# Kernel tuning notes

Measured on AMD Instinct MI355X. Metric: run time of the kernel, lower is better.

## Reference

```python
import jax, jax.numpy as jnp
import numpy as np

TEMPERATURE = 0.5


def setup_inputs() -> dict:
    key = jax.random.key(0)
    k1, k2 = jax.random.split(key)
    N, D = 4096, 512
    emb_i = jax.random.normal(k1, (N, D), dtype=jnp.float32)
    emb_j = jax.random.normal(k2, (N, D), dtype=jnp.float32)
    return {"emb_i": emb_i, "emb_j": emb_j}


def reference(emb_i, emb_j):
    # L2-normalize each embedding row (F.normalize, dim=1)
    z_i = emb_i / jnp.linalg.norm(emb_i, axis=1, keepdims=True)
    z_j = emb_j / jnp.linalg.norm(emb_j, axis=1, keepdims=True)
    reps = jnp.concatenate([z_i, z_j], axis=0)  # [2N, D]
    N = emb_i.shape[0]
    M = 2 * N
    # cosine similarity of normalized vectors == dot product -> [2N, 2N]
    sim = jnp.einsum('id,jd->ij', reps, reps) / TEMPERATURE
    # denominator: sum_k!=i exp(sim[i,k]); original multiplies by one-hot complement
    exp_sim = jnp.exp(sim)
    denom = jnp.sum(exp_sim, axis=1) - jnp.diagonal(exp_sim)  # [2N]
    log_denom = jnp.log(denom)
    # positive pairs: (k, k+N) and (k+N, k)
    idx = jnp.arange(N)
    pos_ij = sim[idx, idx + N]          # sim(k, k+N)/T
    pos_ji = sim[idx + N, idx]          # sim(k+N, k)/T
    loss = jnp.sum(-(pos_ij - log_denom[:N]) - (pos_ji - log_denom[N:]))
    return loss / (2.0 * N)
```

## Files before the change

kernel.cpp:

```cpp
#include <hip/hip_runtime.h>
#include <cstdint>
#include <cstddef>

constexpr int N_ROWS = 4096;
constexpr int D      = 512;
constexpr int M      = 8192;
constexpr int NTILE  = 64;
constexpr int NBLK   = NTILE * (NTILE + 1) / 2;
constexpr int BKB    = 64;
constexpr int NKT    = D / BKB;
constexpr int LDSB   = 128 * BKB;

using f32x16 = __attribute__((ext_vector_type(16))) float;
using i32x4  = __attribute__((ext_vector_type(4))) int;
using i32x8  = __attribute__((ext_vector_type(8))) int;
using ul2    = __attribute__((ext_vector_type(2))) unsigned long;

#define ASYNC_CP16(gsrc, ldst)                                                      \
    __builtin_amdgcn_global_load_lds(                                               \
        (const __attribute__((address_space(1))) unsigned int*)(gsrc),              \
        (__attribute__((address_space(3))) unsigned int*)(ldst), 16, 0, 0)

#define SS_FP8(pk, accum)                                                           \
    do {                                                                            \
        float f0 = __builtin_amdgcn_cvt_f32_fp8((pk), 0);                           \
        float f1 = __builtin_amdgcn_cvt_f32_fp8((pk), 1);                           \
        float f2 = __builtin_amdgcn_cvt_f32_fp8((pk), 2);                           \
        float f3 = __builtin_amdgcn_cvt_f32_fp8((pk), 3);                           \
        (accum) += f0 * f0 + f1 * f1 + f2 * f2 + f3 * f3;                           \
    } while (0)

__global__ __launch_bounds__(256) void normpos_kernel(
    const float* __restrict__ emb_i, const float* __restrict__ emb_j,
    uint8_t* __restrict__ zb, float* __restrict__ diagss,
    float* __restrict__ pos)
{
    const int wave = threadIdx.x >> 6, lane = threadIdx.x & 63;
    const int k = blockIdx.x * 4 + wave;

    const float4* a = (const float4*)(emb_i + (size_t)k * D);
    const float4* b = (const float4*)(emb_j + (size_t)k * D);
    float4 a0 = a[lane * 2], a1 = a[lane * 2 + 1];
    float4 b0 = b[lane * 2], b1 = b[lane * 2 + 1];

    float ssi = a0.x*a0.x + a0.y*a0.y + a0.z*a0.z + a0.w*a0.w
              + a1.x*a1.x + a1.y*a1.y + a1.z*a1.z + a1.w*a1.w;
    float ssj = b0.x*b0.x + b0.y*b0.y + b0.z*b0.z + b0.w*b0.w
              + b1.x*b1.x + b1.y*b1.y + b1.z*b1.z + b1.w*b1.w;
    float dp  = a0.x*b0.x + a0.y*b0.y + a0.z*b0.z + a0.w*b0.w
              + a1.x*b1.x + a1.y*b1.y + a1.z*b1.z + a1.w*b1.w;
    #pragma unroll
    for (int off = 32; off; off >>= 1) {
        ssi += __shfl_xor(ssi, off, 64);
        ssj += __shfl_xor(ssj, off, 64);
        dp  += __shfl_xor(dp,  off, 64);
    }
    const float invi = rsqrtf(ssi), invj = rsqrtf(ssj);

    const float zi[8] = {a0.x*invi, a0.y*invi, a0.z*invi, a0.w*invi,
                         a1.x*invi, a1.y*invi, a1.z*invi, a1.w*invi};
    const float zj[8] = {b0.x*invj, b0.y*invj, b0.z*invj, b0.w*invj,
                         b1.x*invj, b1.y*invj, b1.z*invj, b1.w*invj};

    int pi0 = __builtin_amdgcn_cvt_pk_fp8_f32(zi[0], zi[1], 0, false);
    pi0     = __builtin_amdgcn_cvt_pk_fp8_f32(zi[2], zi[3], pi0, true);
    int pi1 = __builtin_amdgcn_cvt_pk_fp8_f32(zi[4], zi[5], 0, false);
    pi1     = __builtin_amdgcn_cvt_pk_fp8_f32(zi[6], zi[7], pi1, true);
    int pj0 = __builtin_amdgcn_cvt_pk_fp8_f32(zj[0], zj[1], 0, false);
    pj0     = __builtin_amdgcn_cvt_pk_fp8_f32(zj[2], zj[3], pj0, true);
    int pj1 = __builtin_amdgcn_cvt_pk_fp8_f32(zj[4], zj[5], 0, false);
    pj1     = __builtin_amdgcn_cvt_pk_fp8_f32(zj[6], zj[7], pj1, true);

    float dssi = 0.f, dssj = 0.f;
    SS_FP8(pi0, dssi);
    SS_FP8(pi1, dssi);
    SS_FP8(pj0, dssj);
    SS_FP8(pj1, dssj);

    const int x   = (k >> 1) & 3;
    const int sl8 = (lane >> 3) * 8 + ((((lane >> 1) & 3) ^ x) * 2) + (lane & 1);
    const unsigned long long vi =
        ((unsigned long long)(unsigned)pi1 << 32) | (unsigned)pi0;
    const unsigned long long vj =
        ((unsigned long long)(unsigned)pj1 << 32) | (unsigned)pj0;
    *(unsigned long long*)(zb + (size_t)k * D + sl8 * 8)            = vi;
    *(unsigned long long*)(zb + (size_t)(k + N_ROWS) * D + sl8 * 8) = vj;

    #pragma unroll
    for (int off = 32; off; off >>= 1) {
        dssi += __shfl_xor(dssi, off, 64);
        dssj += __shfl_xor(dssj, off, 64);
    }
    if (lane == 0) {
        diagss[k]          = dssi;
        diagss[k + N_ROWS] = dssj;
        pos[k]             = 2.0f * dp * invi * invj;
    }
}

__global__ __launch_bounds__(256, 4) void simgemm_kernel(
    const uint8_t* __restrict__ zb, float* __restrict__ partials)
{
    __shared__ ul2 AsV[2 * LDSB / 16];
    __shared__ ul2 BsV[2 * LDSB / 16];
    __shared__ float rp[4][64];
    __shared__ float cp4[4][64];
    uint8_t* As = (uint8_t*)AsV;
    uint8_t* Bs = (uint8_t*)BsV;

    const int tid  = threadIdx.x;
    const int wave = tid >> 6, lane = tid & 63;
    const int l31  = lane & 31, half = lane >> 5;

    const int t = blockIdx.x;
    int bi = (int)((129.0f - sqrtf(129.0f * 129.0f - 8.0f * (float)t)) * 0.5f);
    while (bi > 0 && bi * (129 - bi) / 2 > t) --bi;
    while ((bi + 1) * (129 - (bi + 1)) / 2 <= t) ++bi;
    const int bj = bi + (t - bi * (129 - bi) / 2);
    const bool diag = (bi == bj);

    const int wrow = (wave >> 1) * 64, wcol = (wave & 1) * 64;

    const int srow = wave * 32 + (lane >> 2);
    const int scol = (lane & 3) * 16;
    const uint8_t* gA = zb + (size_t)(bi * 128 + srow) * D + scol;
    const uint8_t* gB = zb + (size_t)(bj * 128 + srow) * D + scol;
    uint8_t* lA = As + wave * 32 * BKB;
    uint8_t* lB = Bs + wave * 32 * BKB;

#define STAGE4(IT)                                                                  \
    do {                                                                            \
        const int _kc  = (IT) * BKB;                                                \
        const int _off = ((IT) & 1) * LDSB;                                         \
        ASYNC_CP16(gA + _kc,          lA + _off);                                   \
        ASYNC_CP16(gA + _kc + 16 * D, lA + _off + 16 * BKB);                        \
        ASYNC_CP16(gB + _kc,          lB + _off);                                   \
        ASYNC_CP16(gB + _kc + 16 * D, lB + _off + 16 * BKB);                        \
    } while (0)

    STAGE4(0);

    f32x16 acc[2][2] = {};
    const int c0b = ((2 * half) ^ ((l31 >> 1) & 3)) * 16;

    #pragma unroll
    for (int it = 0; it < NKT; ++it) {
        __builtin_amdgcn_s_barrier();
        asm volatile("" ::: "memory");

        if (it + 1 < NKT) {
            STAGE4(it + 1);
            asm volatile("s_waitcnt vmcnt(4)" ::: "memory");
        } else {
            asm volatile("s_waitcnt vmcnt(0)" ::: "memory");
        }
        __builtin_amdgcn_s_barrier();
        asm volatile("" ::: "memory");

        const int cb = (it & 1) * LDSB;
        i32x8 af[2], bf[2];
        #pragma unroll
        for (int f = 0; f < 2; ++f) {
            const uint8_t* pa = As + cb + (size_t)(wrow + f * 32 + l31) * BKB;
            i32x4 alo = *(const i32x4*)(pa + c0b);
            i32x4 ahi = *(const i32x4*)(pa + (c0b ^ 16));
            af[f] = __builtin_shufflevector(alo, ahi, 0, 1, 2, 3, 4, 5, 6, 7);
            const uint8_t* pb = Bs + cb + (size_t)(wcol + f * 32 + l31) * BKB;
            i32x4 blo = *(const i32x4*)(pb + c0b);
            i32x4 bhi = *(const i32x4*)(pb + (c0b ^ 16));
            bf[f] = __builtin_shufflevector(blo, bhi, 0, 1, 2, 3, 4, 5, 6, 7);
        }
        #pragma unroll
        for (int i = 0; i < 2; ++i)
            #pragma unroll
            for (int j = 0; j < 2; ++j)
                acc[i][j] = __builtin_amdgcn_mfma_scale_f32_32x32x64_f8f6f4(
                    af[i], bf[j], acc[i][j], 0, 0,
                    0, 0x7f7f7f7f, 0, 0x7f7f7f7f);
    }

    float rowp[2][16] = {};
    #pragma unroll
    for (int j = 0; j < 2; ++j) {
        float cpj = 0.f;
        #pragma unroll
        for (int i = 0; i < 2; ++i)
            #pragma unroll
            for (int r = 0; r < 16; ++r) {
                float e = __expf(2.0f * acc[i][j][r]);
                rowp[i][r] += e;
                cpj += e;
            }
        if (!diag) {
            cpj += __shfl_xor(cpj, 32, 64);
            if (half == 0) cp4[wave][j * 32 + l31] = cpj;
        }
    }
    #pragma unroll
    for (int i = 0; i < 2; ++i)
        #pragma unroll
        for (int r = 0; r < 16; ++r) {
            float e = rowp[i][r];
            e += __shfl_xor(e, 1, 64);
            e += __shfl_xor(e, 2, 64);
            e += __shfl_xor(e, 4, 64);
            e += __shfl_xor(e, 8, 64);
            e += __shfl_xor(e, 16, 64);
            if (l31 == 0)
                rp[wave][i * 32 + (r & 3) + 8 * (r >> 2) + 4 * half] = e;
        }
    __syncthreads();

    float* pA = partials + (size_t)(bi * NTILE + bj) * 128;
    float* pB = partials + (size_t)(bj * NTILE + bi) * 128;
    if (tid < 128) {
        const int h = tid >> 6, rr = tid & 63;
        pA[tid] = rp[h * 2][rr] + rp[h * 2 + 1][rr];
    } else if (!diag) {
        const int c = tid - 128, h = c >> 6, cc = c & 63;
        pB[c] = cp4[h][cc] + cp4[h + 2][cc];
    }
}

__global__ __launch_bounds__(256) void rowfin_kernel(
    const float* __restrict__ partials, const float* __restrict__ diagss,
    const float* __restrict__ pos, float* __restrict__ lgpart)
{
    const int r  = blockIdx.x;
    const int ri = threadIdx.x & 127;
    const int ch = threadIdx.x >> 7;
    const float* base = partials + (size_t)r * NTILE * 128 + ri;
    float s = 0.f;
    #pragma unroll
    for (int c = 0; c < 32; ++c)
        s += base[(size_t)(ch * 32 + c) * 128];
    __shared__ float half1[128];
    __shared__ float red[4];
    if (ch == 1) half1[ri] = s;
    __syncthreads();
    float lg = 0.f;
    if (ch == 0) {
        float rs = s + half1[ri];
        int row = r * 128 + ri;
        lg = __logf(rs - __expf(2.0f * diagss[row]));
    }
    if (threadIdx.x < 64)
        lg -= 2.0f * pos[r * 64 + threadIdx.x];
    #pragma unroll
    for (int off = 32; off; off >>= 1) lg += __shfl_xor(lg, off, 64);
    const int wave = threadIdx.x >> 6, lane = threadIdx.x & 63;
    if (lane == 0) red[wave] = lg;
    __syncthreads();
    if (threadIdx.x == 0) lgpart[r] = red[0] + red[1] + red[2] + red[3];
}

__global__ __launch_bounds__(64) void loss_kernel(
    const float* __restrict__ lgpart, float* __restrict__ out)
{
    float local = lgpart[threadIdx.x];
    #pragma unroll
    for (int off = 32; off; off >>= 1) local += __shfl_xor(local, off, 64);
    if (threadIdx.x == 0) out[0] = local * (1.0f / 8192.0f);
}

extern "C" void kernel_launch(void* const* d_in, const int* in_sizes, int n_in,
                              void* d_out, int out_size, void* d_ws, size_t ws_size,
                              hipStream_t stream)
{
    const float* emb_i = (const float*)d_in[0];
    const float* emb_j = (const float*)d_in[1];

    uint8_t* zb = (uint8_t*)d_ws;
    float* partials = (float*)((char*)d_ws + (size_t)M * D);
    float* diagss   = partials + (size_t)NTILE * NTILE * 128;
    float* pos      = diagss + M;
    float* lgpart   = pos + N_ROWS;
    float* out      = (float*)d_out;

    normpos_kernel<<<N_ROWS / 4, 256, 0, stream>>>(emb_i, emb_j, zb, diagss, pos);
    simgemm_kernel<<<NBLK, 256, 0, stream>>>(zb, partials);
    rowfin_kernel<<<NTILE, 256, 0, stream>>>(partials, diagss, pos, lgpart);
    loss_kernel<<<1, 64, 0, stream>>>(lgpart, out);
}
```

Baseline: 110.9 us.

## Enlarge similarity GEMM tiles to 256x256 with 8-wave blocks

The symmetric FP8 similarity GEMM moves from 128x128 upper-triangle tiles with 4 waves to 256x256 tiles with 8 waves, each wave computing a 128x64 sub-tile. Larger tiles halve global/LDS traffic per output and cut the block count from 2080 to 528. To keep the existing rowfin partial layout, each 256-wide row sum goes into one 128-column slot and the paired slot is zeroed. The tradeoffs are higher register and LDS use, a 2-block-per-CU occupancy target, and fewer blocks, which may give a coarser tail across CUs.

```diff
diff --git a/kernel.cpp b/kernel.cpp
--- a/kernel.cpp
+++ b/kernel.cpp
@@ -6,10 +6,11 @@
 constexpr int D      = 512;
 constexpr int M      = 8192;
 constexpr int NTILE  = 64;
-constexpr int NBLK   = NTILE * (NTILE + 1) / 2;
+constexpr int NT2    = 32;
+constexpr int NJOB2  = NT2 * (NT2 + 1) / 2;
 constexpr int BKB    = 64;
 constexpr int NKT    = D / BKB;
-constexpr int LDSB   = 128 * BKB;
+constexpr int TBY    = 256 * BKB;
 
 using f32x16 = __attribute__((ext_vector_type(16))) float;
 using i32x4  = __attribute__((ext_vector_type(4))) int;
@@ -98,13 +99,13 @@
     }
 }
 
-__global__ __launch_bounds__(256, 4) void simgemm_kernel(
+__global__ __launch_bounds__(512, 2) void simgemm_kernel(
     const uint8_t* __restrict__ zb, float* __restrict__ partials)
 {
-    __shared__ ul2 AsV[2 * LDSB / 16];
-    __shared__ ul2 BsV[2 * LDSB / 16];
-    __shared__ float rp[4][64];
-    __shared__ float cp4[4][64];
+    __shared__ ul2 AsV[2 * TBY / 16];
+    __shared__ ul2 BsV[2 * TBY / 16];
+    __shared__ float rp[8][128];
+    __shared__ float cp[8][64];
     uint8_t* As = (uint8_t*)AsV;
     uint8_t* Bs = (uint8_t*)BsV;
 
@@ -113,25 +114,28 @@
     const int l31  = lane & 31, half = lane >> 5;
 
     const int t = blockIdx.x;
-    int bi = (int)((129.0f - sqrtf(129.0f * 129.0f - 8.0f * (float)t)) * 0.5f);
-    while (bi > 0 && bi * (129 - bi) / 2 > t) --bi;
-    while ((bi + 1) * (129 - (bi + 1)) / 2 <= t) ++bi;
-    const int bj = bi + (t - bi * (129 - bi) / 2);
+    int bi = (int)((65.0f - sqrtf(4225.0f - 8.0f * (float)t)) * 0.5f);
+    if (bi < 0) bi = 0;
+    if (bi > 31) bi = 31;
+    while (bi > 0 && bi * (65 - bi) / 2 > t) --bi;
+    while ((bi + 1) * (65 - (bi + 1)) / 2 <= t) ++bi;
+    const int bj = bi + (t - bi * (65 - bi) / 2);
     const bool diag = (bi == bj);
 
-    const int wrow = (wave >> 1) * 64, wcol = (wave & 1) * 64;
+    const int wr = wave >> 2, wc = wave & 3;
+    const int wrow = wr * 128, wcol = wc * 64;
 
     const int srow = wave * 32 + (lane >> 2);
     const int scol = (lane & 3) * 16;
-    const uint8_t* gA = zb + (size_t)(bi * 128 + srow) * D + scol;
-    const uint8_t* gB = zb + (size_t)(bj * 128 + srow) * D + scol;
+    const uint8_t* gA = zb + (size_t)(bi * 256 + srow) * D + scol;
+    const uint8_t* gB = zb + (size_t)(bj * 256 + srow) * D + scol;
     uint8_t* lA = As + wave * 32 * BKB;
     uint8_t* lB = Bs + wave * 32 * BKB;
 
 #define STAGE4(IT)                                                                  \
     do {                                                                            \
         const int _kc  = (IT) * BKB;                                                \
-        const int _off = ((IT) & 1) * LDSB;                                         \
+        const int _off = ((IT) & 1) * TBY;                                          \
         ASYNC_CP16(gA + _kc,          lA + _off);                                   \
         ASYNC_CP16(gA + _kc + 16 * D, lA + _off + 16 * BKB);                        \
         ASYNC_CP16(gB + _kc,          lB + _off);                                   \
@@ -140,7 +144,7 @@
 
     STAGE4(0);
 
-    f32x16 acc[2][2] = {};
+    f32x16 acc[4][2] = {};
     const int c0b = ((2 * half) ^ ((l31 >> 1) & 3)) * 16;
 
     #pragma unroll
@@ -157,21 +161,24 @@
         __builtin_amdgcn_s_barrier();
         asm volatile("" ::: "memory");
 
-        const int cb = (it & 1) * LDSB;
-        i32x8 af[2], bf[2];
-        #pragma unroll
-        for (int f = 0; f < 2; ++f) {
+        const int cb = (it & 1) * TBY;
+        i32x8 af[4], bf[2];
+        #pragma unroll
+        for (int f = 0; f < 4; ++f) {
             const uint8_t* pa = As + cb + (size_t)(wrow + f * 32 + l31) * BKB;
             i32x4 alo = *(const i32x4*)(pa + c0b);
             i32x4 ahi = *(const i32x4*)(pa + (c0b ^ 16));
             af[f] = __builtin_shufflevector(alo, ahi, 0, 1, 2, 3, 4, 5, 6, 7);
+        }
+        #pragma unroll
+        for (int f = 0; f < 2; ++f) {
             const uint8_t* pb = Bs + cb + (size_t)(wcol + f * 32 + l31) * BKB;
             i32x4 blo = *(const i32x4*)(pb + c0b);
             i32x4 bhi = *(const i32x4*)(pb + (c0b ^ 16));
             bf[f] = __builtin_shufflevector(blo, bhi, 0, 1, 2, 3, 4, 5, 6, 7);
         }
         #pragma unroll
-        for (int i = 0; i < 2; ++i)
+        for (int i = 0; i < 4; ++i)
             #pragma unroll
             for (int j = 0; j < 2; ++j)
                 acc[i][j] = __builtin_amdgcn_mfma_scale_f32_32x32x64_f8f6f4(
@@ -179,12 +186,12 @@
                     0, 0x7f7f7f7f, 0, 0x7f7f7f7f);
     }
 
-    float rowp[2][16] = {};
+    float rowp[4][16] = {};
     #pragma unroll
     for (int j = 0; j < 2; ++j) {
         float cpj = 0.f;
         #pragma unroll
-        for (int i = 0; i < 2; ++i)
+        for (int i = 0; i < 4; ++i)
             #pragma unroll
             for (int r = 0; r < 16; ++r) {
                 float e = __expf(2.0f * acc[i][j][r]);
@@ -193,11 +200,11 @@
             }
         if (!diag) {
             cpj += __shfl_xor(cpj, 32, 64);
-            if (half == 0) cp4[wave][j * 32 + l31] = cpj;
-        }
-    }
-    #pragma unroll
-    for (int i = 0; i < 2; ++i)
+            if (half == 0) cp[wave][j * 32 + l31] = cpj;
+        }
+    }
+    #pragma unroll
+    for (int i = 0; i < 4; ++i)
         #pragma unroll
         for (int r = 0; r < 16; ++r) {
             float e = rowp[i][r];
@@ -211,14 +218,20 @@
         }
     __syncthreads();
 
-    float* pA = partials + (size_t)(bi * NTILE + bj) * 128;
-    float* pB = partials + (size_t)(bj * NTILE + bi) * 128;
-    if (tid < 128) {
-        const int h = tid >> 6, rr = tid & 63;
-        pA[tid] = rp[h * 2][rr] + rp[h * 2 + 1][rr];
+    if (tid < 256) {
+        const int rh = tid >> 7, rl = tid & 127;
+        const int wb = rh * 4;
+        const float v = rp[wb][rl] + rp[wb + 1][rl] + rp[wb + 2][rl] + rp[wb + 3][rl];
+        const size_t rc = (size_t)(2 * bi + rh);
+        partials[(rc * NTILE + 2 * bj)     * 128 + rl] = v;
+        partials[(rc * NTILE + 2 * bj + 1) * 128 + rl] = 0.f;
     } else if (!diag) {
-        const int c = tid - 128, h = c >> 6, cc = c & 63;
-        pB[c] = cp4[h][cc] + cp4[h + 2][cc];
+        const int c = tid - 256;
+        const int wcq = c >> 6, cl = c & 63;
+        const float v = cp[wcq][cl] + cp[wcq + 4][cl];
+        const size_t rc = (size_t)(2 * bj + (c >> 7));
+        partials[(rc * NTILE + 2 * bi)     * 128 + (c & 127)] = v;
+        partials[(rc * NTILE + 2 * bi + 1) * 128 + (c & 127)] = 0.f;
     }
 }
 
@@ -278,7 +291,7 @@
     float* out      = (float*)d_out;
 
     normpos_kernel<<<N_ROWS / 4, 256, 0, stream>>>(emb_i, emb_j, zb, diagss, pos);
-    simgemm_kernel<<<NBLK, 256, 0, stream>>>(zb, partials);
+    simgemm_kernel<<<NJOB2, 512, 0, stream>>>(zb, partials);
     rowfin_kernel<<<NTILE, 256, 0, stream>>>(partials, diagss, pos, lgpart);
     loss_kernel<<<1, 64, 0, stream>>>(lgpart, out);
 }
```

Measured after the change: 133.6 us. 1.2x slower.
